# Kernel tuning notes

Hardware: AMD Instinct MI355X
Metric: run time of the kernel (lower is better)

The kernel has to match this reference:

```python
import jax, jax.numpy as jnp
import numpy as np

N_NODES = 50000
N_EDGES = 1600000
S_FEAT, F_FEAT, HID, HEADS = 100, 200, 256, 8
HEAD_DIM = HID // HEADS


def setup_inputs() -> dict:
    key = jax.random.key(0)
    ks = jax.random.split(key, 8)
    inp = {
        "x": jax.random.normal(ks[0], (N_NODES, S_FEAT + F_FEAT), dtype=jnp.float32),
        "edge_index": jax.random.randint(ks[1], (2, N_EDGES), 0, N_NODES, dtype=jnp.int64),
        "W_s": jax.random.normal(ks[2], (S_FEAT, HID), dtype=jnp.float32) * (1.0 / np.sqrt(S_FEAT)),
        "b_s": jnp.zeros((HID,), jnp.float32),
        "W_f": jax.random.normal(ks[3], (F_FEAT, HID), dtype=jnp.float32) * (1.0 / np.sqrt(F_FEAT)),
        "b_f": jnp.zeros((HID,), jnp.float32),
        "in_proj_w": jax.random.normal(ks[4], (3 * HID, HID), dtype=jnp.float32) * (1.0 / np.sqrt(HID)),
        "in_proj_b": jnp.zeros((3 * HID,), jnp.float32),
        "out_proj_w": jax.random.normal(ks[5], (HID, HID), dtype=jnp.float32) * (1.0 / np.sqrt(HID)),
        "out_proj_b": jnp.zeros((HID,), jnp.float32),
        "out_w": jax.random.normal(ks[6], (1, HID), dtype=jnp.float32) * (1.0 / np.sqrt(HID)),
        "out_b": jnp.zeros((1,), jnp.float32),
    }
    return inp


def _gcn_conv(feat, W, b, src, dst, deg_inv, coef, n):
    # PyG GCNConv: h = feat @ W; out[i] = sum_j norm_ij * h_j + (1/deg_i) * h_i + b
    h = feat @ W  # [N, HID]
    agg = jax.ops.segment_sum(coef[:, None] * h[src], dst, num_segments=n)
    return agg + deg_inv[:, None] * h + b


def reference(x, edge_index, W_s, b_s, W_f, b_f,
              in_proj_w, in_proj_b, out_proj_w, out_proj_b, out_w, out_b):
    n = x.shape[0]
    src, dst = edge_index[0], edge_index[1]
    # symmetric GCN normalization with self-loops (edge weight 1)
    deg = 1.0 + jax.ops.segment_sum(jnp.ones(src.shape[0], x.dtype), dst, num_segments=n)
    deg_inv_sqrt = jax.lax.rsqrt(deg)
    coef = deg_inv_sqrt[src] * deg_inv_sqrt[dst]  # [E]
    deg_inv = deg_inv_sqrt * deg_inv_sqrt         # self-loop norm = 1/deg

    s = jax.nn.relu(_gcn_conv(x[:, :S_FEAT], W_s, b_s, src, dst, deg_inv, coef, n))
    f = jax.nn.relu(_gcn_conv(x[:, S_FEAT:S_FEAT + F_FEAT], W_f, b_f, src, dst, deg_inv, coef, n))

    comb = jnp.stack([s, f], axis=1)  # [N, 2, HID]
    qkv = comb @ in_proj_w.T + in_proj_b  # [N, 2, 3*HID]
    q, k, v = jnp.split(qkv, 3, axis=-1)
    def heads(t):  # [N, 2, HID] -> [N, H, 2, Dh]
        return t.reshape(n, 2, HEADS, HEAD_DIM).transpose(0, 2, 1, 3)
    q, k, v = heads(q), heads(k), heads(v)
    scores = jnp.einsum('nhqd,nhkd->nhqk', q, k) / np.sqrt(HEAD_DIM)
    attn = jax.nn.softmax(scores, axis=-1)
    o = jnp.einsum('nhqk,nhkd->nhqd', attn, v).transpose(0, 2, 1, 3).reshape(n, 2, HID)
    o = o @ out_proj_w.T + out_proj_b  # [N, 2, HID]

    fused = o.mean(axis=1)                 # [N, HID]
    pooled = fused.mean(axis=0, keepdims=True)  # [1, HID] (global_mean_pool, one graph)
    return (pooled @ out_w.T + out_b).squeeze(-1)  # [1]
```

## Files before the change

kernel.cpp:

```cpp
#include <hip/hip_runtime.h>
#include <hip/hip_bf16.h>
#include <math.h>

#define N_NODES 50000
#define N_EDGES 1600000
#define M_ROWS  100000

static const size_t XB_OFF   = 0;
static const size_t Y_OFF    = 32000000;
static const size_t CSR_OFF  = 64000000;
static const size_t C_OFF    = 0;
static const size_t COMB_OFF = 104000000;
static const size_t ROW_OFF  = 155200000;
static const size_t CNT_OFF  = 155400064;
static const size_t CUR_OFF  = 155600128;
static const size_t DIS_OFF  = 155800192;
static const size_t DINV_OFF = 156000256;
static const size_t BT_OFF   = 156200320;
static const size_t B2_OFF   = 156495232;
static const size_t WP_OFF   = 156497536;
static const size_t U_OFF    = 156498560;
static const size_t CH_OFF   = 156506752;
static const size_t FLAG_OFF = 156506816;
static const size_t ACC_OFF  = 156506880;
static const size_t WT2_OFF  = 156506944;
static const size_t WS_NEED  = 156834624;

typedef __attribute__((ext_vector_type(8))) short short8v;
typedef __attribute__((ext_vector_type(4))) float f32x4;

__device__ __forceinline__ float bf_lo(unsigned int u) { return __uint_as_float(u << 16); }
__device__ __forceinline__ float bf_hi(unsigned int u) { return __uint_as_float(u & 0xffff0000u); }
__device__ __forceinline__ unsigned short f2bf(float f) {
    unsigned int x = __float_as_uint(f);
    return (unsigned short)((x + 0x7fffu + ((x >> 16) & 1u)) >> 16);
}


__global__ void k_guard(float* out) { if (threadIdx.x == 0) out[0] = -12345.0f; }

__global__ void k_detect(const int* __restrict__ raw, int* __restrict__ flag) {
    if (raw[2 * threadIdx.x + 1] != 0) atomicOr(flag, 1);
}

__device__ __forceinline__ void load_edge(const int* raw, int is32, int e, int& s, int& d) {
    if (is32) { s = raw[e]; d = raw[N_EDGES + e]; }
    else      { s = raw[2 * (size_t)e]; d = raw[2 * ((size_t)N_EDGES + e)]; }
}

__global__ __launch_bounds__(256) void k_deg(const int* __restrict__ raw,
                                             const int* __restrict__ flag,
                                             int* __restrict__ cnt) {
    int e = blockIdx.x * 256 + threadIdx.x;
    if (e >= N_EDGES) return;
    int s, d; load_edge(raw, *flag, e, s, d);
    atomicAdd(&cnt[d], 1);
}

__global__ __launch_bounds__(256) void k_norm(const int* __restrict__ cnt,
                                              float* __restrict__ dis, float* __restrict__ dinv) {
    int n = blockIdx.x * 256 + threadIdx.x;
    if (n < N_NODES) {
        float d = 1.0f + (float)cnt[n];
        float r = rsqrtf(d);
        dis[n]  = r;
        dinv[n] = r * r;
    }
}

__global__ __launch_bounds__(1024) void k_scan(const int* __restrict__ cnt,
                                               int* __restrict__ rowptr) {
    __shared__ int part[1024];
    const int CH = 49;
    int tid = threadIdx.x;
    int base = tid * CH;
    int s = 0;
    for (int i = 0; i < CH; ++i) {
        int idx = base + i;
        if (idx < N_NODES) s += cnt[idx];
    }
    part[tid] = s;
    __syncthreads();
    for (int off = 1; off < 1024; off <<= 1) {
        int v = (tid >= off) ? part[tid - off] : 0;
        __syncthreads();
        part[tid] += v;
        __syncthreads();
    }
    int excl = (tid == 0) ? 0 : part[tid - 1];
    for (int i = 0; i < CH; ++i) {
        int idx = base + i;
        if (idx < N_NODES) { rowptr[idx] = excl; excl += cnt[idx]; }
    }
    if (tid == 1023) rowptr[N_NODES] = excl;
}

__global__ __launch_bounds__(256) void k_place(const int* __restrict__ raw,
                                               const int* __restrict__ flag,
                                               const int* __restrict__ rowptr,
                                               int* __restrict__ cur,
                                               int* __restrict__ csr) {
    int e = blockIdx.x * 256 + threadIdx.x;
    if (e >= N_EDGES) return;
    int s, d; load_edge(raw, *flag, e, s, d);
    int pos = rowptr[d] + atomicAdd(&cur[d], 1);
    csr[pos] = s;
}

__global__ __launch_bounds__(256) void k_cvtx(const float* __restrict__ x,
                                              unsigned short* __restrict__ xb) {
    int idx = blockIdx.x * 256 + threadIdx.x;
    int row = idx / 80, g = idx - row * 80;
    if (row >= N_NODES) return;
    int c0 = g * 4;
    ushort4 o;
    if (c0 < 300) {
        float4 v = *reinterpret_cast<const float4*>(x + (size_t)row * 300 + c0);
        o.x = f2bf(v.x); o.y = f2bf(v.y); o.z = f2bf(v.z); o.w = f2bf(v.w);
    } else {
        o = make_ushort4(0, 0, 0, 0);
    }
    *reinterpret_cast<ushort4*>(xb + (size_t)row * 320 + c0) = o;
}

__global__ __launch_bounds__(256) void k_wt2(const float* __restrict__ Ws,
                                             const float* __restrict__ Wf,
                                             unsigned short* __restrict__ Wt2) {
    int j = blockIdx.x;
    for (int k = threadIdx.x; k < 320; k += 256) {
        float v = 0.0f;
        if (j < 256) { if (k < 100) v = Ws[(size_t)k * 256 + j]; }
        else         { if (k >= 100 && k < 300) v = Wf[(size_t)(k - 100) * 256 + (j - 256)]; }
        Wt2[(size_t)j * 320 + k] = f2bf(v);
    }
}

__global__ __launch_bounds__(256) void k_aggx(const int* __restrict__ csr,
                                              const int* __restrict__ rowptr,
                                              const float* __restrict__ dis,
                                              const float* __restrict__ dinv,
                                              const unsigned short* __restrict__ xb,
                                              unsigned short* __restrict__ y) {
    int n    = blockIdx.x * 4 + (threadIdx.x >> 6);
    int lane = threadIdx.x & 63;
    if (n >= N_NODES || lane >= 40) return;
    int beg = rowptr[n], end = rowptr[n + 1];
    float a0=0,a1=0,a2=0,a3=0,a4=0,a5=0,a6=0,a7=0;
    for (int e = beg; e < end; ++e) {
        int s = csr[e];
        float c = dis[s];
        uint4 v = *reinterpret_cast<const uint4*>(xb + (size_t)s * 320 + lane * 8);
        a0 += c * bf_lo(v.x); a1 += c * bf_hi(v.x);
        a2 += c * bf_lo(v.y); a3 += c * bf_hi(v.y);
        a4 += c * bf_lo(v.z); a5 += c * bf_hi(v.z);
        a6 += c * bf_lo(v.w); a7 += c * bf_hi(v.w);
    }
    float dn = dis[n], di = dinv[n];
    uint4 hv = *reinterpret_cast<const uint4*>(xb + (size_t)n * 320 + lane * 8);
    float r0 = dn*a0 + di*bf_lo(hv.x);
    float r1 = dn*a1 + di*bf_hi(hv.x);
    float r2 = dn*a2 + di*bf_lo(hv.y);
    float r3 = dn*a3 + di*bf_hi(hv.y);
    float r4 = dn*a4 + di*bf_lo(hv.z);
    float r5 = dn*a5 + di*bf_hi(hv.z);
    float r6 = dn*a6 + di*bf_lo(hv.w);
    float r7 = dn*a7 + di*bf_hi(hv.w);
    uint4 o;
    o.x = (unsigned int)f2bf(r0) | ((unsigned int)f2bf(r1) << 16);
    o.y = (unsigned int)f2bf(r2) | ((unsigned int)f2bf(r3) << 16);
    o.z = (unsigned int)f2bf(r4) | ((unsigned int)f2bf(r5) << 16);
    o.w = (unsigned int)f2bf(r6) | ((unsigned int)f2bf(r7) << 16);
    *reinterpret_cast<uint4*>(y + (size_t)n * 320 + lane * 8) = o;
}

__global__ __launch_bounds__(256) void k_comb(const unsigned short* __restrict__ y,
                                              const unsigned short* __restrict__ Wt2,
                                              const float* __restrict__ bs,
                                              const float* __restrict__ bf,
                                              unsigned short* __restrict__ comb) {
    __shared__ __align__(16) unsigned short sA[64][40];
    __shared__ __align__(16) unsigned short sB[64][40];
    int tid  = threadIdx.x;
    int lane = tid & 63, wid = tid >> 6;
    int wm = wid >> 1, wn = wid & 1;
    int arow = tid >> 2, aseg = (tid & 3) * 8;
    int cblk = blockIdx.x, rblk = blockIdx.y;
    long grow = (long)rblk * 64 + arow;
    bool aval = grow < N_NODES;
    const unsigned short* aptr = y + grow * 320 + aseg;
    const unsigned short* bptr = Wt2 + ((long)cblk * 64 + arow) * 320 + aseg;

    f32x4 acc00 = {0,0,0,0}, acc01 = {0,0,0,0}, acc10 = {0,0,0,0}, acc11 = {0,0,0,0};
    int fr = lane & 15, fk = (lane >> 4) * 8;

    for (int ks = 0; ks < 10; ++ks) {
        uint4 av = aval ? *reinterpret_cast<const uint4*>(aptr + ks * 32) : make_uint4(0,0,0,0);
        uint4 bv = *reinterpret_cast<const uint4*>(bptr + ks * 32);
        __syncthreads();
        *reinterpret_cast<uint4*>(&sA[arow][aseg]) = av;
        *reinterpret_cast<uint4*>(&sB[arow][aseg]) = bv;
        __syncthreads();
        short8v a0 = *reinterpret_cast<const short8v*>(&sA[wm * 32 + fr][fk]);
        short8v a1 = *reinterpret_cast<const short8v*>(&sA[wm * 32 + 16 + fr][fk]);
        short8v b0 = *reinterpret_cast<const short8v*>(&sB[wn * 32 + fr][fk]);
        short8v b1 = *reinterpret_cast<const short8v*>(&sB[wn * 32 + 16 + fr][fk]);
        acc00 = __builtin_amdgcn_mfma_f32_16x16x32_bf16(a0, b0, acc00, 0, 0, 0);
        acc01 = __builtin_amdgcn_mfma_f32_16x16x32_bf16(a0, b1, acc01, 0, 0, 0);
        acc10 = __builtin_amdgcn_mfma_f32_16x16x32_bf16(a1, b0, acc10, 0, 0, 0);
        acc11 = __builtin_amdgcn_mfma_f32_16x16x32_bf16(a1, b1, acc11, 0, 0, 0);
    }

    int crow = rblk * 64 + wm * 32;
    int ccol = cblk * 64 + wn * 32;
    int rb = (lane >> 4) * 4;
    #pragma unroll
    for (int mn = 0; mn < 4; ++mn) {
        int m = mn >> 1, nn = mn & 1;
        f32x4 a = (mn == 0) ? acc00 : (mn == 1) ? acc01 : (mn == 2) ? acc10 : acc11;
        int col = ccol + nn * 16 + (lane & 15);
        int t  = col >> 8;
        int c2 = col & 255;
        float bias = t ? bf[c2] : bs[c2];
        #pragma unroll
        for (int j = 0; j < 4; ++j) {
            int row = crow + m * 16 + rb + j;
            if (row < N_NODES)
                comb[(size_t)(2 * row + t) * 256 + c2] = f2bf(fmaxf(a[j] + bias, 0.0f));
        }
    }
}

__global__ __launch_bounds__(256) void k_wprime(const float* __restrict__ ow,
                                                const float* __restrict__ opw,
                                                float* __restrict__ wp) {
    int i = threadIdx.x;
    float s = 0.0f;
    for (int j = 0; j < 256; ++j) s += ow[j] * opw[j * 256 + i];
    wp[i] = s;
}

__global__ __launch_bounds__(256) void k_u(const float* __restrict__ ipw,
                                           const float* __restrict__ ipb,
                                           const float* __restrict__ wp,
                                           float* __restrict__ u, float* __restrict__ ch) {
    int hd = blockIdx.x, i = threadIdx.x;
    float s = 0.0f;
    for (int d = 0; d < 32; ++d)
        s += ipw[(size_t)(512 + hd * 32 + d) * 256 + i] * wp[hd * 32 + d];
    u[hd * 256 + i] = s;
    if (i == 0) {
        float c = 0.0f;
        for (int d = 0; d < 32; ++d) c += ipb[512 + hd * 32 + d] * wp[hd * 32 + d];
        ch[hd] = c;
    }
}

__global__ __launch_bounds__(256) void k_makeB(const float* __restrict__ ipw,
                                               const float* __restrict__ ipb,
                                               const float* __restrict__ u,
                                               const float* __restrict__ ch,
                                               unsigned short* __restrict__ Bt,
                                               float* __restrict__ b2) {
    int j = blockIdx.x, k = threadIdx.x;
    float v = 0.0f;
    if (j < 512)      v = ipw[(size_t)j * 256 + k];
    else if (j < 520) v = u[(j - 512) * 256 + k];
    Bt[(size_t)j * 256 + k] = f2bf(v);
    if (k == 0) b2[j] = (j < 512) ? ipb[j] : ((j < 520) ? ch[j - 512] : 0.0f);
}

__global__ __launch_bounds__(256) void k_qkv(const unsigned short* __restrict__ comb,
                                             const unsigned short* __restrict__ Bt,
                                             const float* __restrict__ b2,
                                             unsigned short* __restrict__ C) {
    __shared__ __align__(16) unsigned short sA[64][40];
    __shared__ __align__(16) unsigned short sB[64][40];
    int tid  = threadIdx.x;
    int lane = tid & 63, wid = tid >> 6;
    int wm = wid >> 1, wn = wid & 1;
    int arow = tid >> 2, aseg = (tid & 3) * 8;
    int cblk = blockIdx.x, rblk = blockIdx.y;
    long grow = (long)rblk * 64 + arow;
    bool aval = grow < M_ROWS;
    const unsigned short* aptr = comb + grow * 256 + aseg;
    const unsigned short* bptr = Bt + ((long)cblk * 64 + arow) * 256 + aseg;

    f32x4 acc00 = {0,0,0,0}, acc01 = {0,0,0,0}, acc10 = {0,0,0,0}, acc11 = {0,0,0,0};
    int fr = lane & 15, fk = (lane >> 4) * 8;

    for (int ks = 0; ks < 8; ++ks) {
        uint4 av = aval ? *reinterpret_cast<const uint4*>(aptr + ks * 32) : make_uint4(0,0,0,0);
        uint4 bv = *reinterpret_cast<const uint4*>(bptr + ks * 32);
        __syncthreads();
        *reinterpret_cast<uint4*>(&sA[arow][aseg]) = av;
        *reinterpret_cast<uint4*>(&sB[arow][aseg]) = bv;
        __syncthreads();
        short8v a0 = *reinterpret_cast<const short8v*>(&sA[wm * 32 + fr][fk]);
        short8v a1 = *reinterpret_cast<const short8v*>(&sA[wm * 32 + 16 + fr][fk]);
        short8v b0 = *reinterpret_cast<const short8v*>(&sB[wn * 32 + fr][fk]);
        short8v b1 = *reinterpret_cast<const short8v*>(&sB[wn * 32 + 16 + fr][fk]);
        acc00 = __builtin_amdgcn_mfma_f32_16x16x32_bf16(a0, b0, acc00, 0, 0, 0);
        acc01 = __builtin_amdgcn_mfma_f32_16x16x32_bf16(a0, b1, acc01, 0, 0, 0);
        acc10 = __builtin_amdgcn_mfma_f32_16x16x32_bf16(a1, b0, acc10, 0, 0, 0);
        acc11 = __builtin_amdgcn_mfma_f32_16x16x32_bf16(a1, b1, acc11, 0, 0, 0);
    }

    int crow = rblk * 64 + wm * 32;
    int ccol = cblk * 64 + wn * 32;
    int rb = (lane >> 4) * 4;
    #pragma unroll
    for (int mn = 0; mn < 4; ++mn) {
        int m = mn >> 1, nn = mn & 1;
        f32x4 a = (mn == 0) ? acc00 : (mn == 1) ? acc01 : (mn == 2) ? acc10 : acc11;
        int col = ccol + nn * 16 + (lane & 15);
        if (col < 520) {
            float bias = b2[col];
            #pragma unroll
            for (int j = 0; j < 4; ++j) {
                int row = crow + m * 16 + rb + j;
                if (row < M_ROWS) C[(size_t)row * 520 + col] = f2bf(a[j] + bias);
            }
        }
    }
}

__global__ __launch_bounds__(256) void k_att(const unsigned short* __restrict__ C,
                                             double* __restrict__ accum) {
    __shared__ float sQK[4][2][536];
    __shared__ float red[4];
    int tid = threadIdx.x;
    int lane = tid & 63, wid = tid >> 6;
    int n = blockIdx.x * 4 + wid;

    if (n < N_NODES) {
        for (int c = lane; c < 130; c += 64) {
            int r = (c >= 65), co = c - r * 65;
            int off = co * 8;
            uint4 v = *reinterpret_cast<const uint4*>(C + ((size_t)(2 * n + r) * 520 + off));
            float f0 = bf_lo(v.x), f1 = bf_hi(v.x), f2 = bf_lo(v.y), f3 = bf_hi(v.y);
            float f4 = bf_lo(v.z), f5 = bf_hi(v.z), f6 = bf_lo(v.w), f7 = bf_hi(v.w);
            float* dst = &sQK[wid][r][0];
            dst[(off+0) + ((off+0)>>5)] = f0; dst[(off+1) + ((off+1)>>5)] = f1;
            dst[(off+2) + ((off+2)>>5)] = f2; dst[(off+3) + ((off+3)>>5)] = f3;
            dst[(off+4) + ((off+4)>>5)] = f4; dst[(off+5) + ((off+5)>>5)] = f5;
            dst[(off+6) + ((off+6)>>5)] = f6; dst[(off+7) + ((off+7)>>5)] = f7;
        }
    }
    __syncthreads();

    float acc = 0.0f;
    if (lane < 32 && n < N_NODES) {
        int hd = lane >> 2, t = (lane >> 1) & 1, t2 = lane & 1;
        const float* Q  = &sQK[wid][t][0];
        const float* K2 = &sQK[wid][t2][0];
        int qb = 33 * hd;
        int kb = 264 + 33 * hd;
        float s = 0.0f;
        #pragma unroll 8
        for (int d = 0; d < 32; ++d) s += Q[qb + d] * K2[kb + d];
        s *= 0.17677669529663687f;
        float so = __shfl_xor(s, 1);
        float m  = fmaxf(s, so);
        float e  = expf(s - m), eo = expf(so - m);
        float w  = e / (e + eo);
        acc = w * K2[528 + hd];
    }
    #pragma unroll
    for (int off = 1; off < 32; off <<= 1) acc += __shfl_xor(acc, off);
    if (lane == 0) red[wid] = acc;
    __syncthreads();
    if (tid == 0) atomicAdd(accum, (double)(red[0] + red[1] + red[2] + red[3]));
}

__global__ __launch_bounds__(256) void k_final(const float* __restrict__ ow,
                                               const float* __restrict__ opb,
                                               const float* __restrict__ ob,
                                               const double* __restrict__ accum,
                                               float* __restrict__ out) {
    __shared__ float red[256];
    int tid = threadIdx.x;
    red[tid] = ow[tid] * opb[tid];
    __syncthreads();
    for (int s = 128; s > 0; s >>= 1) {
        if (tid < s) red[tid] += red[tid + s];
        __syncthreads();
    }
    if (tid == 0)
        out[0] = (float)(accum[0] / (2.0 * N_NODES) + (double)red[0] + (double)ob[0]);
}

extern "C" void kernel_launch(void* const* d_in, const int* in_sizes, int n_in,
                              void* d_out, int out_size, void* d_ws, size_t ws_size,
                              hipStream_t stream) {
    const float* x   = (const float*)d_in[0];
    const int*   ei  = (const int*)d_in[1];
    const float* Ws  = (const float*)d_in[2];
    const float* bs  = (const float*)d_in[3];
    const float* Wf  = (const float*)d_in[4];
    const float* bf  = (const float*)d_in[5];
    const float* ipw = (const float*)d_in[6];
    const float* ipb = (const float*)d_in[7];
    const float* opw = (const float*)d_in[8];
    const float* opb = (const float*)d_in[9];
    const float* ow  = (const float*)d_in[10];
    const float* ob  = (const float*)d_in[11];
    float* out = (float*)d_out;

    if (ws_size < WS_NEED) { k_guard<<<1, 64, 0, stream>>>(out); return; }

    char* ws = (char*)d_ws;
    unsigned short* xb   = (unsigned short*)(ws + XB_OFF);
    unsigned short* y    = (unsigned short*)(ws + Y_OFF);
    int*            csr  = (int*)           (ws + CSR_OFF);
    unsigned short* C    = (unsigned short*)(ws + C_OFF);
    unsigned short* comb = (unsigned short*)(ws + COMB_OFF);
    int*            row  = (int*)           (ws + ROW_OFF);
    int*            cnt  = (int*)           (ws + CNT_OFF);
    int*            cur  = (int*)           (ws + CUR_OFF);
    float*          dis  = (float*)         (ws + DIS_OFF);
    float*          dinv = (float*)         (ws + DINV_OFF);
    unsigned short* Bt   = (unsigned short*)(ws + BT_OFF);
    float*          b2   = (float*)         (ws + B2_OFF);
    float*          wp   = (float*)         (ws + WP_OFF);
    float*          u    = (float*)         (ws + U_OFF);
    float*          chv  = (float*)         (ws + CH_OFF);
    int*            flag = (int*)           (ws + FLAG_OFF);
    double*         accum= (double*)        (ws + ACC_OFF);
    unsigned short* Wt2  = (unsigned short*)(ws + WT2_OFF);

    hipMemsetAsync(cnt,   0, (size_t)N_NODES * 4, stream);
    hipMemsetAsync(cur,   0, (size_t)N_NODES * 4, stream);
    hipMemsetAsync(flag,  0, 4, stream);
    hipMemsetAsync(accum, 0, 8, stream);

    k_detect<<<1, 256, 0, stream>>>(ei, flag);
    k_deg   <<<(N_EDGES + 255) / 256, 256, 0, stream>>>(ei, flag, cnt);
    k_norm  <<<(N_NODES + 255) / 256, 256, 0, stream>>>(cnt, dis, dinv);
    k_scan  <<<1, 1024, 0, stream>>>(cnt, row);
    k_place <<<(N_EDGES + 255) / 256, 256, 0, stream>>>(ei, flag, row, cur, csr);

    k_cvtx<<<(N_NODES * 80 + 255) / 256, 256, 0, stream>>>(x, xb);
    k_wt2 <<<512, 256, 0, stream>>>(Ws, Wf, Wt2);

    k_aggx<<<(N_NODES + 3) / 4, 256, 0, stream>>>(csr, row, dis, dinv, xb, y);

    k_wprime<<<1,   256, 0, stream>>>(ow, opw, wp);
    k_u     <<<8,   256, 0, stream>>>(ipw, ipb, wp, u, chv);
    k_makeB <<<576, 256, 0, stream>>>(ipw, ipb, u, chv, Bt, b2);

    dim3 gc(8, (N_NODES + 63) / 64);
    k_comb<<<gc, 256, 0, stream>>>(y, Wt2, bs, bf, comb);

    dim3 gq(9, (M_ROWS + 63) / 64);
    k_qkv<<<gq, 256, 0, stream>>>(comb, Bt, b2, C);

    k_att<<<(N_NODES + 3) / 4, 256, 0, stream>>>(C, accum);
    k_final<<<1, 256, 0, stream>>>(ow, opb, ob, accum, out);
}
```

Measured before the change: 874.4 us.

## Fuse QKV GEMM with per-node attention reduction and unroll edge aggregation

Merges the QKV GEMM and the attention kernel into one kernel. Each block computes all 9 column tiles for 64 rows into a padded LDS tile, then runs the 2-token softmax and reduction straight from LDS. This removes the round trip of the 100000x520 bf16 intermediate through global memory and one launch. The cost is large LDS use per block (~70KB), which cuts occupancy, and a serial loop over column tiles with the A tile reloaded each time. Separately, the edge-aggregation loop is unrolled by four to put more gather loads in flight at once.

```diff
diff --git a/kernel.cpp b/kernel.cpp
--- a/kernel.cpp
+++ b/kernel.cpp
@@ -9,7 +9,6 @@
 static const size_t XB_OFF   = 0;
 static const size_t Y_OFF    = 32000000;
 static const size_t CSR_OFF  = 64000000;
-static const size_t C_OFF    = 0;
 static const size_t COMB_OFF = 104000000;
 static const size_t ROW_OFF  = 155200000;
 static const size_t CNT_OFF  = 155400064;
@@ -31,6 +30,7 @@
 
 __device__ __forceinline__ float bf_lo(unsigned int u) { return __uint_as_float(u << 16); }
 __device__ __forceinline__ float bf_hi(unsigned int u) { return __uint_as_float(u & 0xffff0000u); }
+__device__ __forceinline__ float bf2f(unsigned short u) { return __uint_as_float((unsigned int)u << 16); }
 __device__ __forceinline__ unsigned short f2bf(float f) {
     unsigned int x = __float_as_uint(f);
     return (unsigned short)((x + 0x7fffu + ((x >> 16) & 1u)) >> 16);
@@ -146,14 +146,29 @@
     if (n >= N_NODES || lane >= 40) return;
     int beg = rowptr[n], end = rowptr[n + 1];
     float a0=0,a1=0,a2=0,a3=0,a4=0,a5=0,a6=0,a7=0;
-    for (int e = beg; e < end; ++e) {
+    int e = beg;
+    for (; e + 4 <= end; e += 4) {
+        int s0 = csr[e], s1 = csr[e+1], s2 = csr[e+2], s3 = csr[e+3];
+        float c0 = dis[s0], c1 = dis[s1], c2 = dis[s2], c3 = dis[s3];
+        uint4 v0 = *reinterpret_cast<const uint4*>(xb + (size_t)s0 * 320 + lane * 8);
+        uint4 v1 = *reinterpret_cast<const uint4*>(xb + (size_t)s1 * 320 + lane * 8);
+        uint4 v2 = *reinterpret_cast<const uint4*>(xb + (size_t)s2 * 320 + lane * 8);
+        uint4 v3 = *reinterpret_cast<const uint4*>(xb + (size_t)s3 * 320 + lane * 8);
+        a0 += c0*bf_lo(v0.x); a1 += c0*bf_hi(v0.x); a2 += c0*bf_lo(v0.y); a3 += c0*bf_hi(v0.y);
+        a4 += c0*bf_lo(v0.z); a5 += c0*bf_hi(v0.z); a6 += c0*bf_lo(v0.w); a7 += c0*bf_hi(v0.w);
+        a0 += c1*bf_lo(v1.x); a1 += c1*bf_hi(v1.x); a2 += c1*bf_lo(v1.y); a3 += c1*bf_hi(v1.y);
+        a4 += c1*bf_lo(v1.z); a5 += c1*bf_hi(v1.z); a6 += c1*bf_lo(v1.w); a7 += c1*bf_hi(v1.w);
+        a0 += c2*bf_lo(v2.x); a1 += c2*bf_hi(v2.x); a2 += c2*bf_lo(v2.y); a3 += c2*bf_hi(v2.y);
+        a4 += c2*bf_lo(v2.z); a5 += c2*bf_hi(v2.z); a6 += c2*bf_lo(v2.w); a7 += c2*bf_hi(v2.w);
+        a0 += c3*bf_lo(v3.x); a1 += c3*bf_hi(v3.x); a2 += c3*bf_lo(v3.y); a3 += c3*bf_hi(v3.y);
+        a4 += c3*bf_lo(v3.z); a5 += c3*bf_hi(v3.z); a6 += c3*bf_lo(v3.w); a7 += c3*bf_hi(v3.w);
+    }
+    for (; e < end; ++e) {
         int s = csr[e];
         float c = dis[s];
         uint4 v = *reinterpret_cast<const uint4*>(xb + (size_t)s * 320 + lane * 8);
-        a0 += c * bf_lo(v.x); a1 += c * bf_hi(v.x);
-        a2 += c * bf_lo(v.y); a3 += c * bf_hi(v.y);
-        a4 += c * bf_lo(v.z); a5 += c * bf_hi(v.z);
-        a6 += c * bf_lo(v.w); a7 += c * bf_hi(v.w);
+        a0 += c*bf_lo(v.x); a1 += c*bf_hi(v.x); a2 += c*bf_lo(v.y); a3 += c*bf_hi(v.y);
+        a4 += c*bf_lo(v.z); a5 += c*bf_hi(v.z); a6 += c*bf_lo(v.w); a7 += c*bf_hi(v.w);
     }
     float dn = dis[n], di = dinv[n];
     uint4 hv = *reinterpret_cast<const uint4*>(xb + (size_t)n * 320 + lane * 8);
@@ -269,107 +284,98 @@
     if (k == 0) b2[j] = (j < 512) ? ipb[j] : ((j < 520) ? ch[j - 512] : 0.0f);
 }
 
-__global__ __launch_bounds__(256) void k_qkv(const unsigned short* __restrict__ comb,
-                                             const unsigned short* __restrict__ Bt,
-                                             const float* __restrict__ b2,
-                                             unsigned short* __restrict__ C) {
+__global__ __launch_bounds__(256) void k_fuse(const unsigned short* __restrict__ comb,
+                                              const unsigned short* __restrict__ Bt,
+                                              const float* __restrict__ b2,
+                                              double* __restrict__ accum) {
+    __shared__ __align__(16) unsigned short CT[64][544];
     __shared__ __align__(16) unsigned short sA[64][40];
     __shared__ __align__(16) unsigned short sB[64][40];
+    __shared__ float red[256];
+
     int tid  = threadIdx.x;
     int lane = tid & 63, wid = tid >> 6;
     int wm = wid >> 1, wn = wid & 1;
     int arow = tid >> 2, aseg = (tid & 3) * 8;
-    int cblk = blockIdx.x, rblk = blockIdx.y;
-    long grow = (long)rblk * 64 + arow;
+    long grow = (long)blockIdx.x * 64 + arow;
     bool aval = grow < M_ROWS;
     const unsigned short* aptr = comb + grow * 256 + aseg;
-    const unsigned short* bptr = Bt + ((long)cblk * 64 + arow) * 256 + aseg;
-
-    f32x4 acc00 = {0,0,0,0}, acc01 = {0,0,0,0}, acc10 = {0,0,0,0}, acc11 = {0,0,0,0};
     int fr = lane & 15, fk = (lane >> 4) * 8;
-
-    for (int ks = 0; ks < 8; ++ks) {
-        uint4 av = aval ? *reinterpret_cast<const uint4*>(aptr + ks * 32) : make_uint4(0,0,0,0);
-        uint4 bv = *reinterpret_cast<const uint4*>(bptr + ks * 32);
-        __syncthreads();
-        *reinterpret_cast<uint4*>(&sA[arow][aseg]) = av;
-        *reinterpret_cast<uint4*>(&sB[arow][aseg]) = bv;
-        __syncthreads();
-        short8v a0 = *reinterpret_cast<const short8v*>(&sA[wm * 32 + fr][fk]);
-        short8v a1 = *reinterpret_cast<const short8v*>(&sA[wm * 32 + 16 + fr][fk]);
-        short8v b0 = *reinterpret_cast<const short8v*>(&sB[wn * 32 + fr][fk]);
-        short8v b1 = *reinterpret_cast<const short8v*>(&sB[wn * 32 + 16 + fr][fk]);
-        acc00 = __builtin_amdgcn_mfma_f32_16x16x32_bf16(a0, b0, acc00, 0, 0, 0);
-        acc01 = __builtin_amdgcn_mfma_f32_16x16x32_bf16(a0, b1, acc01, 0, 0, 0);
-        acc10 = __builtin_amdgcn_mfma_f32_16x16x32_bf16(a1, b0, acc10, 0, 0, 0);
-        acc11 = __builtin_amdgcn_mfma_f32_16x16x32_bf16(a1, b1, acc11, 0, 0, 0);
-    }
-
-    int crow = rblk * 64 + wm * 32;
-    int ccol = cblk * 64 + wn * 32;
     int rb = (lane >> 4) * 4;
-    #pragma unroll
-    for (int mn = 0; mn < 4; ++mn) {
-        int m = mn >> 1, nn = mn & 1;
-        f32x4 a = (mn == 0) ? acc00 : (mn == 1) ? acc01 : (mn == 2) ? acc10 : acc11;
-        int col = ccol + nn * 16 + (lane & 15);
-        if (col < 520) {
-            float bias = b2[col];
-            #pragma unroll
-            for (int j = 0; j < 4; ++j) {
-                int row = crow + m * 16 + rb + j;
-                if (row < M_ROWS) C[(size_t)row * 520 + col] = f2bf(a[j] + bias);
+
+    for (int cb = 0; cb < 9; ++cb) {
+        const unsigned short* bptr = Bt + ((long)cb * 64 + arow) * 256 + aseg;
+        f32x4 acc00 = {0,0,0,0}, acc01 = {0,0,0,0}, acc10 = {0,0,0,0}, acc11 = {0,0,0,0};
+        for (int ks = 0; ks < 8; ++ks) {
+            uint4 av = aval ? *reinterpret_cast<const uint4*>(aptr + ks * 32) : make_uint4(0,0,0,0);
+            uint4 bv = *reinterpret_cast<const uint4*>(bptr + ks * 32);
+            __syncthreads();
+            *reinterpret_cast<uint4*>(&sA[arow][aseg]) = av;
+            *reinterpret_cast<uint4*>(&sB[arow][aseg]) = bv;
+            __syncthreads();
+            short8v a0 = *reinterpret_cast<const short8v*>(&sA[wm * 32 + fr][fk]);
+            short8v a1 = *reinterpret_cast<const short8v*>(&sA[wm * 32 + 16 + fr][fk]);
+            short8v b0 = *reinterpret_cast<const short8v*>(&sB[wn * 32 + fr][fk]);
+            short8v b1 = *reinterpret_cast<const short8v*>(&sB[wn * 32 + 16 + fr][fk]);
+            acc00 = __builtin_amdgcn_mfma_f32_16x16x32_bf16(a0, b0, acc00, 0, 0, 0);
+            acc01 = __builtin_amdgcn_mfma_f32_16x16x32_bf16(a0, b1, acc01, 0, 0, 0);
+            acc10 = __builtin_amdgcn_mfma_f32_16x16x32_bf16(a1, b0, acc10, 0, 0, 0);
+            acc11 = __builtin_amdgcn_mfma_f32_16x16x32_bf16(a1, b1, acc11, 0, 0, 0);
+        }
+        int ccol = cb * 64 + wn * 32;
+        #pragma unroll
+        for (int mn = 0; mn < 4; ++mn) {
+            int m = mn >> 1, nn = mn & 1;
+            f32x4 a = (mn == 0) ? acc00 : (mn == 1) ? acc01 : (mn == 2) ? acc10 : acc11;
+            int col = ccol + nn * 16 + (lane & 15);
+            if (col < 520) {
+                float bias = b2[col];
+                int pcol = col + (col >> 5);
+                #pragma unroll
+                for (int j = 0; j < 4; ++j)
+                    CT[wm * 32 + m * 16 + rb + j][pcol] = f2bf(a[j] + bias);
             }
         }
     }
-}
-
-__global__ __launch_bounds__(256) void k_att(const unsigned short* __restrict__ C,
-                                             double* __restrict__ accum) {
-    __shared__ float sQK[4][2][536];
-    __shared__ float red[4];
-    int tid = threadIdx.x;
-    int lane = tid & 63, wid = tid >> 6;
-    int n = blockIdx.x * 4 + wid;
-
-    if (n < N_NODES) {
-        for (int c = lane; c < 130; c += 64) {
-            int r = (c >= 65), co = c - r * 65;
-            int off = co * 8;
-            uint4 v = *reinterpret_cast<const uint4*>(C + ((size_t)(2 * n + r) * 520 + off));
-            float f0 = bf_lo(v.x), f1 = bf_hi(v.x), f2 = bf_lo(v.y), f3 = bf_hi(v.y);
-            float f4 = bf_lo(v.z), f5 = bf_hi(v.z), f6 = bf_lo(v.w), f7 = bf_hi(v.w);
-            float* dst = &sQK[wid][r][0];
-            dst[(off+0) + ((off+0)>>5)] = f0; dst[(off+1) + ((off+1)>>5)] = f1;
-            dst[(off+2) + ((off+2)>>5)] = f2; dst[(off+3) + ((off+3)>>5)] = f3;
-            dst[(off+4) + ((off+4)>>5)] = f4; dst[(off+5) + ((off+5)>>5)] = f5;
-            dst[(off+6) + ((off+6)>>5)] = f6; dst[(off+7) + ((off+7)>>5)] = f7;
+    __syncthreads();
+
+    float acc = 0.0f;
+    #pragma unroll
+    for (int ii = 0; ii < 2; ++ii) {
+        int it = tid + ii * 256;
+        int node32 = it >> 4;
+        int rem = it & 15, hd = rem >> 1, t = rem & 1;
+        int gnode = blockIdx.x * 32 + node32;
+        if (gnode < N_NODES) {
+            const unsigned short* qr = &CT[2 * node32 + t][0];
+            const unsigned short* k0 = &CT[2 * node32 + 0][0];
+            const unsigned short* k1 = &CT[2 * node32 + 1][0];
+            int qb = hd * 32 + hd;
+            int kb = 256 + hd * 32 + 8 + hd;
+            float s0 = 0.0f, s1 = 0.0f;
+            #pragma unroll 8
+            for (int d = 0; d < 32; ++d) {
+                float qv = bf2f(qr[qb + d]);
+                s0 += qv * bf2f(k0[kb + d]);
+                s1 += qv * bf2f(k1[kb + d]);
+            }
+            const float sc = 0.17677669529663687f;
+            s0 *= sc; s1 *= sc;
+            float m = fmaxf(s0, s1);
+            float e0 = expf(s0 - m), e1 = expf(s1 - m);
+            float inv = 1.0f / (e0 + e1);
+            float vw0 = bf2f(k0[528 + hd]);
+            float vw1 = bf2f(k1[528 + hd]);
+            acc += (e0 * vw0 + e1 * vw1) * inv;
         }
     }
+    red[tid] = acc;
     __syncthreads();
-
-    float acc = 0.0f;
-    if (lane < 32 && n < N_NODES) {
-        int hd = lane >> 2, t = (lane >> 1) & 1, t2 = lane & 1;
-        const float* Q  = &sQK[wid][t][0];
-        const float* K2 = &sQK[wid][t2][0];
-        int qb = 33 * hd;
-        int kb = 264 + 33 * hd;
-        float s = 0.0f;
-        #pragma unroll 8
-        for (int d = 0; d < 32; ++d) s += Q[qb + d] * K2[kb + d];
-        s *= 0.17677669529663687f;
-        float so = __shfl_xor(s, 1);
-        float m  = fmaxf(s, so);
-        float e  = expf(s - m), eo = expf(so - m);
-        float w  = e / (e + eo);
-        acc = w * K2[528 + hd];
-    }
-    #pragma unroll
-    for (int off = 1; off < 32; off <<= 1) acc += __shfl_xor(acc, off);
-    if (lane == 0) red[wid] = acc;
-    __syncthreads();
-    if (tid == 0) atomicAdd(accum, (double)(red[0] + red[1] + red[2] + red[3]));
+    for (int s = 128; s > 0; s >>= 1) {
+        if (tid < s) red[tid] += red[tid + s];
+        __syncthreads();
+    }
+    if (tid == 0) atomicAdd(accum, (double)red[0]);
 }
 
 __global__ __launch_bounds__(256) void k_final(const float* __restrict__ ow,
@@ -412,7 +418,6 @@
     unsigned short* xb   = (unsigned short*)(ws + XB_OFF);
     unsigned short* y    = (unsigned short*)(ws + Y_OFF);
     int*            csr  = (int*)           (ws + CSR_OFF);
-    unsigned short* C    = (unsigned short*)(ws + C_OFF);
     unsigned short* comb = (unsigned short*)(ws + COMB_OFF);
     int*            row  = (int*)           (ws + ROW_OFF);
     int*            cnt  = (int*)           (ws + CNT_OFF);
@@ -451,9 +456,6 @@
     dim3 gc(8, (N_NODES + 63) / 64);
     k_comb<<<gc, 256, 0, stream>>>(y, Wt2, bs, bf, comb);
 
-    dim3 gq(9, (M_ROWS + 63) / 64);
-    k_qkv<<<gq, 256, 0, stream>>>(comb, Bt, b2, C);
-
-    k_att<<<(N_NODES + 3) / 4, 256, 0, stream>>>(C, accum);
+    k_fuse<<<(M_ROWS + 63) / 64, 256, 0, stream>>>(comb, Bt, b2, accum);
     k_final<<<1, 256, 0, stream>>>(ow, opb, ob, accum, out);
 }
```

After: 714.6 us. 1.22x faster.
